# Performance work log

Measured on AMD Instinct MI355X. Metric: run time of the kernel, lower is better.

## Reference

```python
import jax, jax.numpy as jnp
import numpy as np

N = 50000      # entity nodes
E = 300000     # edges in edge_index_all (and edge_index)
E_LINE = 50000 # line-graph edges over relations
EH = 128       # e_hidden
RH = 64        # r_hidden
REL1 = 2000
REL2 = 2000
GH = 3 * EH + RH  # GAT hidden = 448


def seg_softmax(e, idx, n):
    # torch_geometric softmax: exp(e - segmax[idx]) / (segsum + 1e-16)
    m = jax.ops.segment_max(e, idx, num_segments=n)
    ex = jnp.exp(e - m[idx])
    s = jax.ops.segment_sum(ex, idx, num_segments=n)
    return ex / (s[idx] + 1e-16)


def setup_inputs() -> dict:
    key = jax.random.key(0)
    ks = jax.random.split(key, 24)

    def nrm(k, shape, s=0.1):
        return jax.random.normal(k, shape, dtype=jnp.float32) * s

    # edges without self loops: dst = (src + off) % N, off in [1, N)
    src = jax.random.randint(ks[0], (E,), 0, N)
    off = jax.random.randint(ks[1], (E,), 1, N)
    edge_index_all = jnp.stack([src, (src + off) % N])
    src2 = jax.random.randint(ks[2], (E,), 0, N)
    off2 = jax.random.randint(ks[3], (E,), 1, N)
    edge_index = jnp.stack([src2, (src2 + off2) % N])

    rel = jax.random.randint(ks[4], (E,), 0, REL1)
    rel_all = jax.random.randint(ks[5], (E,), 0, 2 * REL1)
    line_graph_index_out = jax.random.randint(ks[6], (2, E_LINE), 0, REL1)
    line_graph_index_in = jax.random.randint(ks[7], (2, E_LINE), 0, REL1)

    return {
        "x_e": nrm(ks[8], (N, EH), 1.0),
        "rel_emb1": nrm(ks[9], (REL1, RH), 1.0),
        "rel_emb2": nrm(ks[10], (REL2, RH), 1.0),
        "w_gcn1": nrm(ks[11], (EH, EH)),
        "Wh1": nrm(ks[12], (EH, EH)),
        "bh1": nrm(ks[13], (EH,)),
        "w_gcn2": nrm(ks[14], (EH, EH)),
        "Wh2": nrm(ks[15], (EH, EH)),
        "bh2": nrm(ks[16], (EH,)),
        "ai_l": nrm(ks[17], (RH,)),
        "aj_l": nrm(ks[18], (RH,)),
        "w_tw": nrm(ks[19], (2 * EH + RH,)),
        "ai_g": nrm(ks[20], (GH,)),
        "aj_g": nrm(ks[21], (GH,)),
        "ar_g": nrm(ks[22], (RH,)),
        "edge_index": edge_index,
        "rel": rel,
        "edge_index_all": edge_index_all,
        "rel_all": rel_all,
        "line_graph_index_out": line_graph_index_out,
        "line_graph_index_in": line_graph_index_in,
    }


def mrea_forward(x_e, rel_emb1, w_gcn1, Wh1, bh1, w_gcn2, Wh2, bh2,
                 ai_l, aj_l, w_tw, ai_g, aj_g, ar_g,
                 edge_index_all, rel_all, lg_out, lg_in):
    n = x_e.shape[0]
    # GCN/GAT unpack: edge_index_j, edge_index_i = edge_index (row0=j, row1=i)
    j, i = edge_index_all[0], edge_index_all[1]

    def gcn(x, W):
        deg = jax.ops.segment_sum(jnp.ones(i.shape, x.dtype), i, num_segments=n)
        dinv = jnp.where(deg > 0, deg ** -0.5, 0.0)
        norm = dinv[j] * dinv[i]  # [E]
        agg = jax.nn.relu(jax.ops.segment_sum(norm[:, None] * x[j], i, num_segments=n))
        return agg @ W.T

    def highway(x1, x2, W, b):
        g = jax.nn.sigmoid(x1 @ W.T + b)
        return g * x2 + (1.0 - g) * x1

    x = highway(x_e, gcn(x_e, w_gcn1), Wh1, bh1)
    x = highway(x, gcn(x, w_gcn2), Wh2, bh2)

    # L_GAT over relation line graphs (softmax grouped by edge_index_j, as in source)
    nr = rel_emb1.shape[0]
    def l_gat(xr, ei):
        jj, ii = ei[0], ei[1]
        e = (xr @ ai_l)[ii] + (xr @ aj_l)[jj]
        alpha = seg_softmax(jax.nn.leaky_relu(e), jj, nr)
        return jax.nn.relu(jax.ops.segment_sum(alpha[:, None] * xr[jj], ii, num_segments=nr))

    rel_emb = jnp.concatenate([l_gat(rel_emb1, lg_out), l_gat(rel_emb1, lg_in)], axis=0)  # [2*REL1, RH]

    # T-wise attention: edge_index_i, edge_index_j = edge_index_all (row0=i, row1=j)
    ti, tj = edge_index_all[0], edge_index_all[1]
    feat = jnp.concatenate([x[ti], rel_emb[rel_all], x[tj]], axis=1)  # [E, 2e+r]
    att = seg_softmax(feat @ w_tw, ti, n)
    x_agg = jax.nn.relu(jax.ops.segment_sum(feat * att[:, None], ti, num_segments=n))
    x_rel = jnp.concatenate([x, x_agg], axis=1)  # [N, 3e+r]

    # GAT on x_rel with relation bias (row0=j, row1=i)
    e = (x_rel @ ai_g)[i] + (x_rel @ aj_g)[j] + (rel_emb @ ar_g)[rel_all]
    alpha = seg_softmax(jax.nn.leaky_relu(e), i, n)
    gat_out = jax.nn.relu(jax.ops.segment_sum(alpha[:, None] * x_rel[j], i, num_segments=n))

    return jnp.concatenate([x_rel, gat_out], axis=1)  # [N, 2*(3e+r)]


def reference(x_e, rel_emb1, rel_emb2, w_gcn1, Wh1, bh1, w_gcn2, Wh2, bh2,
              ai_l, aj_l, w_tw, ai_g, aj_g, ar_g,
              edge_index, rel, edge_index_all, rel_all,
              line_graph_index_out, line_graph_index_in):
    # Branch rel.max()+1 == rel1_size is true for our data -> rel_emb1 used.
    # rel_emb2, edge_index, rel do not enter the computation on this branch.
    return mrea_forward(x_e, rel_emb1, w_gcn1, Wh1, bh1, w_gcn2, Wh2, bh2,
                        ai_l, aj_l, w_tw, ai_g, aj_g, ar_g,
                        edge_index_all, rel_all,
                        line_graph_index_out, line_graph_index_in)
```

## Files before the change

kernel.cpp:

```cpp
#include <hip/hip_runtime.h>
#include <math.h>

#define NN 50000
#define EE 300000
#define EL 50000
#define EH 128
#define RH 64
#define R1 2000
#define NR2 4000
#define OD 896
#define NT64 782
#define GCNB 12500
#define CAP 32
#define LGCAP 64

using f32x4 = __attribute__((ext_vector_type(4))) float;
using bf16x8 = __attribute__((ext_vector_type(8))) short;

__device__ __forceinline__ float leaky(float x) { return x >= 0.f ? x : 0.01f * x; }

__device__ __forceinline__ void atomicMaxF(float* addr, float val) {
    if (val >= 0.f) atomicMax((int*)addr, __float_as_int(val));
    else            atomicMin((unsigned int*)addr, __float_as_uint(val));
}

__device__ __forceinline__ short bfrn(float f) {
    unsigned u = __float_as_uint(f);
    return (short)((u + 0x7FFFu + ((u >> 16) & 1u)) >> 16);
}
__device__ __forceinline__ void cvt1(float f, short& h, short& l) {
    h = bfrn(f);
    float hf = __uint_as_float(((unsigned)(unsigned short)h) << 16);
    l = bfrn(f - hf);
}
__device__ __forceinline__ void cvt8(float4 a, float4 b, bf16x8& hi, bf16x8& lo) {
    float v[8] = {a.x, a.y, a.z, a.w, b.x, b.y, b.z, b.w};
#pragma unroll
    for (int e = 0; e < 8; ++e) {
        short h, l;
        cvt1(v[e], h, l);
        hi[e] = h;
        lo[e] = l;
    }
}

__global__ __launch_bounds__(256) void k_pre(const float* __restrict__ W0, const float* __restrict__ W1,
                                             const float* __restrict__ W2, const float* __restrict__ W3,
                                             float* __restrict__ P0, float* __restrict__ P1,
                                             float* __restrict__ P2, float* __restrict__ P3,
                                             const float* __restrict__ rel1,
                                             const float* __restrict__ ai_l, const float* __restrict__ aj_l,
                                             float* __restrict__ s_i, float* __restrict__ s_j,
                                             float* __restrict__ lgmax) {
    int b = blockIdx.x, tid = threadIdx.x;
    if (b < 32) {
        int slot = b * 256 + tid;
        int m = slot >> 11;
        int rem = slot & 2047;
        int kb = rem >> 9;
        int nt = (rem >> 6) & 7;
        int l = rem & 63;
        const float* W = m == 0 ? W0 : m == 1 ? W1 : m == 2 ? W2 : W3;
        float* P = m == 0 ? P0 : m == 1 ? P1 : m == 2 ? P2 : P3;
        int n = (nt << 4) + (l & 15);
        int k0 = (kb << 5) + ((l >> 4) << 2);
        float4 a0 = *(const float4*)(W + (n << 7) + k0);
        float4 a1 = *(const float4*)(W + (n << 7) + k0 + 16);
        bf16x8 hv, lv;
        cvt8(a0, a1, hv, lv);
        int u = ((kb << 3) + nt) * 64 + l;
        *(bf16x8*)(P + ((long)u << 2)) = hv;
        *(bf16x8*)(P + 8192 + ((long)u << 2)) = lv;
        return;
    }
    if (b < 40) {
        int r = (b - 32) * 256 + tid;
        if (r < R1) {
            const float* m = rel1 + (long)r * 64;
            float a = 0.f, bb = 0.f;
#pragma unroll
            for (int c = 0; c < 64; ++c) {
                float v = m[c];
                a += v * ai_l[c];
                bb += v * aj_l[c];
            }
            s_i[r] = a;
            s_j[r] = bb;
        }
        return;
    }
    int g = (b - 40) * 256 + tid;
    if (g < 2 * R1) lgmax[g] = -INFINITY;
}

__global__ void k_fill_all(const int* __restrict__ e0, const int* __restrict__ e1,
                           const int* __restrict__ rel_all,
                           int* __restrict__ cnt0, int* __restrict__ cnt1,
                           int2* __restrict__ csr0p, int2* __restrict__ csr1p,
                           const int* __restrict__ lgo, const int* __restrict__ lgi,
                           const float* __restrict__ s_i, const float* __restrict__ s_j,
                           float* __restrict__ lgsc, float* __restrict__ lgmax,
                           int* __restrict__ lgcnt, int* __restrict__ lgsrc,
                           int* __restrict__ lgpos) {
    int gid = blockIdx.x * blockDim.x + threadIdx.x;
    int stride = gridDim.x * blockDim.x;
    for (int i = gid; i < EE; i += stride) {
        int j0 = e0[i], i1 = e1[i], ra = rel_all[i];
        int p = atomicAdd(&cnt0[j0], 1);
        if (p < CAP) csr0p[(j0 << 5) + p] = make_int2(i1, ra);
        int q = atomicAdd(&cnt1[i1], 1);
        if (q < CAP) csr1p[(i1 << 5) + q] = make_int2(j0, ra);
    }
    for (int e = gid; e < 2 * EL; e += stride) {
        int g1 = e >= EL;
        int ee = g1 ? e - EL : e;
        const int* L = g1 ? lgi : lgo;
        int jj = L[ee], ii = L[ee + EL];
        float v = leaky(s_j[jj] + s_i[ii]);
        lgsc[e] = v;
        atomicMaxF(&lgmax[(g1 ? R1 : 0) + jj], v);
        int g = (g1 ? R1 : 0) + ii;
        int p = atomicAdd(&lgcnt[g], 1);
        if (p < LGCAP) {
            lgsrc[(g << 6) + p] = jj;
            lgpos[e] = (g << 6) + p;
        } else {
            lgpos[e] = -1;
        }
    }
}

__global__ __launch_bounds__(256) void k_dinv(const int* __restrict__ cnt1, float* __restrict__ dinv) {
    int i = blockIdx.x * 256 + threadIdx.x;
    if (i < NN) {
        int v = cnt1[i];
        dinv[i] = v > 0 ? rsqrtf((float)v) : 0.f;
    }
}

template <bool RELU>
__device__ __forceinline__ void mfma_phase(const float* __restrict__ A, const float* __restrict__ P,
                                           float4* lds4, int tid, int l, int arow, f32x4 (&acc)[8]) {
#pragma unroll
    for (int s = 0; s < 2; ++s) {
        const float* Ap = A + ((long)arow << 7) + (s << 6) + ((l >> 4) << 2);
        float4 a0 = *(const float4*)(Ap);
        float4 a1 = *(const float4*)(Ap + 16);
        float4 a2 = *(const float4*)(Ap + 32);
        float4 a3 = *(const float4*)(Ap + 48);
        if (RELU) {
            a0.x = fmaxf(a0.x, 0.f); a0.y = fmaxf(a0.y, 0.f); a0.z = fmaxf(a0.z, 0.f); a0.w = fmaxf(a0.w, 0.f);
            a1.x = fmaxf(a1.x, 0.f); a1.y = fmaxf(a1.y, 0.f); a1.z = fmaxf(a1.z, 0.f); a1.w = fmaxf(a1.w, 0.f);
            a2.x = fmaxf(a2.x, 0.f); a2.y = fmaxf(a2.y, 0.f); a2.z = fmaxf(a2.z, 0.f); a2.w = fmaxf(a2.w, 0.f);
            a3.x = fmaxf(a3.x, 0.f); a3.y = fmaxf(a3.y, 0.f); a3.z = fmaxf(a3.z, 0.f); a3.w = fmaxf(a3.w, 0.f);
        }
        __syncthreads();
        const float4* srcH = (const float4*)P + (s << 10);
        const float4* srcL = (const float4*)P + 2048 + (s << 10);
#pragma unroll
        for (int i = 0; i < 4; ++i) {
            lds4[(i << 8) + tid] = srcH[(i << 8) + tid];
            lds4[1024 + (i << 8) + tid] = srcL[(i << 8) + tid];
        }
        __syncthreads();
        bf16x8 ah0, al0, ah1, al1;
        cvt8(a0, a1, ah0, al0);
        cvt8(a2, a3, ah1, al1);
        const bf16x8* BH = (const bf16x8*)lds4;
        const bf16x8* BL = BH + 1024;
#pragma unroll
        for (int nt = 0; nt < 8; ++nt) {
            bf16x8 bh0 = BH[(nt << 6) + l];
            bf16x8 bl0 = BL[(nt << 6) + l];
            bf16x8 bh1 = BH[512 + (nt << 6) + l];
            bf16x8 bl1 = BL[512 + (nt << 6) + l];
            f32x4 c = acc[nt];
            c = __builtin_amdgcn_mfma_f32_16x16x32_bf16(ah0, bh0, c, 0, 0, 0);
            c = __builtin_amdgcn_mfma_f32_16x16x32_bf16(al0, bh0, c, 0, 0, 0);
            c = __builtin_amdgcn_mfma_f32_16x16x32_bf16(ah0, bl0, c, 0, 0, 0);
            c = __builtin_amdgcn_mfma_f32_16x16x32_bf16(ah1, bh1, c, 0, 0, 0);
            c = __builtin_amdgcn_mfma_f32_16x16x32_bf16(al1, bh1, c, 0, 0, 0);
            c = __builtin_amdgcn_mfma_f32_16x16x32_bf16(ah1, bl1, c, 0, 0, 0);
            acc[nt] = c;
        }
    }
}

template <bool XB>
__global__ __launch_bounds__(256) void k_gcn_mfma(const float* __restrict__ Agg, const float* __restrict__ Xin,
                                                  float* __restrict__ Xout,
                                                  const float* __restrict__ Pg, const float* __restrict__ Ph,
                                                  const float* __restrict__ b,
                                                  const float* __restrict__ wtw192, float* __restrict__ xb) {
    __shared__ float4 lds4[2048];
    const int tid = threadIdx.x;
    const int l = tid & 63;
    const int wv = tid >> 6;
    const int l15 = l & 15;
    const int l4 = l >> 4;
    const int rowbase = blockIdx.x * 64 + (wv << 4);
    int arow = rowbase + l15;
    if (arow >= NN) arow = NN - 1;
    f32x4 tAcc[8], hAcc[8];
#pragma unroll
    for (int nt = 0; nt < 8; ++nt) {
        tAcc[nt] = {0.f, 0.f, 0.f, 0.f};
        hAcc[nt] = {0.f, 0.f, 0.f, 0.f};
    }
    mfma_phase<true>(Agg, Pg, lds4, tid, l, arow, tAcc);
    mfma_phase<false>(Xin, Ph, lds4, tid, l, arow, hAcc);
    const int r0 = rowbase + (l4 << 2);
    float xbp[4] = {0.f, 0.f, 0.f, 0.f};
#pragma unroll
    for (int nt = 0; nt < 8; ++nt) {
        float bv = b[(nt << 4) + l15];
#pragma unroll
        for (int r = 0; r < 4; ++r) {
            int row = r0 + r;
            if (row < NN) {
                long off = ((long)row << 7) + (nt << 4) + l15;
                float xv = Xin[off];
                float g = 1.f / (1.f + expf(-(hAcc[nt][r] + bv)));
                float ov = g * tAcc[nt][r] + (1.f - g) * xv;
                Xout[off] = ov;
                if (XB) xbp[r] += ov * wtw192[(nt << 4) + l15];
            }
        }
    }
    if (XB) {
#pragma unroll
        for (int r = 0; r < 4; ++r) {
#pragma unroll
            for (int off = 1; off < 16; off <<= 1) xbp[r] += __shfl_xor(xbp[r], off);
            int row = r0 + r;
            if (l15 == 0 && row < NN) xb[row] = xbp[r];
        }
    }
}

template <int MODE>
__global__ __launch_bounds__(256) void k_gcn_gather(const int2* __restrict__ csr1p, const int* __restrict__ cnt1,
                                                    const float* __restrict__ dinv,
                                                    const float* __restrict__ x, float* __restrict__ agg,
                                                    const int* __restrict__ lgo, const int* __restrict__ lgi,
                                                    const float* __restrict__ lgsc, const float* __restrict__ lgmax,
                                                    float* __restrict__ lgsum,
                                                    const int* __restrict__ lgpos, float* __restrict__ lgscp,
                                                    const int* __restrict__ lgcnt, const int* __restrict__ lgsrc,
                                                    const float* __restrict__ rel1, float* __restrict__ relemb,
                                                    const float* __restrict__ wtw, const float* __restrict__ arg,
                                                    float* __restrict__ rw, float* __restrict__ gr) {
    if (blockIdx.x < GCNB) {
        int w = blockIdx.x * 4 + (threadIdx.x >> 6);
        int lane = threadIdx.x & 63;
        int deg = cnt1[w];
        if (deg > CAP) deg = CAP;
        int b = w << 5, en = b + deg;
        float dd = dinv[w];
        const float2* x2 = (const float2*)x;
        float2 aA = {0.f, 0.f}, aB = {0.f, 0.f}, aC = {0.f, 0.f}, aD = {0.f, 0.f};
        int idx = b;
        for (; idx + 3 < en; idx += 4) {
            int s0 = csr1p[idx].x, s1 = csr1p[idx + 1].x;
            int s2 = csr1p[idx + 2].x, s3 = csr1p[idx + 3].x;
            float w0 = dinv[s0] * dd, w1 = dinv[s1] * dd;
            float w2 = dinv[s2] * dd, w3 = dinv[s3] * dd;
            float2 v0 = x2[((long)s0 << 6) + lane];
            float2 v1 = x2[((long)s1 << 6) + lane];
            float2 v2 = x2[((long)s2 << 6) + lane];
            float2 v3 = x2[((long)s3 << 6) + lane];
            aA.x += w0 * v0.x; aA.y += w0 * v0.y;
            aB.x += w1 * v1.x; aB.y += w1 * v1.y;
            aC.x += w2 * v2.x; aC.y += w2 * v2.y;
            aD.x += w3 * v3.x; aD.y += w3 * v3.y;
        }
        for (; idx < en; ++idx) {
            int s = csr1p[idx].x;
            float w0 = dinv[s] * dd;
            float2 v0 = x2[((long)s << 6) + lane];
            aA.x += w0 * v0.x; aA.y += w0 * v0.y;
        }
        float2 r;
        r.x = (aA.x + aB.x) + (aC.x + aD.x);
        r.y = (aA.y + aB.y) + (aC.y + aD.y);
        ((float2*)agg)[((long)w << 6) + lane] = r;
        return;
    }
    if (MODE == 1) {
        int gid = (blockIdx.x - GCNB) * 256 + threadIdx.x;
        const int stride = 391 * 256;
        for (int e = gid; e < 2 * EL; e += stride) {
            int g1 = e >= EL;
            int ee = g1 ? e - EL : e;
            const int* L = g1 ? lgi : lgo;
            int jjg = (g1 ? R1 : 0) + L[ee];
            float ex = expf(lgsc[e] - lgmax[jjg]);
            int lp = lgpos[e];
            if (lp >= 0) lgscp[lp] = ex;
            atomicAdd(&lgsum[jjg], ex);
        }
    } else {
        int d = (blockIdx.x - GCNB) * 4 + (threadIdx.x >> 6);
        int lane = threadIdx.x & 63;
        if (d >= NR2) return;
        int base = d >= R1 ? R1 : 0;
        int deg = lgcnt[d];
        if (deg > LGCAP) deg = LGCAP;
        int b = d << 6, en = b + deg;
        float aA = 0.f, aB = 0.f;
        int idx = b;
        for (; idx + 1 < en; idx += 2) {
            int j0 = lgsrc[idx], j1 = lgsrc[idx + 1];
            float al0 = lgscp[idx] / (lgsum[base + j0] + 1e-16f);
            float al1 = lgscp[idx + 1] / (lgsum[base + j1] + 1e-16f);
            aA += al0 * rel1[((long)j0 << 6) + lane];
            aB += al1 * rel1[((long)j1 << 6) + lane];
        }
        if (idx < en) {
            int j0 = lgsrc[idx];
            aA += (lgscp[idx] / (lgsum[base + j0] + 1e-16f)) * rel1[((long)j0 << 6) + lane];
        }
        float v = fmaxf(aA + aB, 0.f);
        relemb[((long)d << 6) + lane] = v;
        float pa = v * wtw[128 + lane];
        float pb = v * arg[lane];
        for (int off = 32; off > 0; off >>= 1) {
            pa += __shfl_down(pa, off);
            pb += __shfl_down(pb, off);
        }
        if (lane == 0) { rw[d] = pa; gr[d] = pb; }
    }
}

__global__ __launch_bounds__(256) void k_tw_gather(const int2* __restrict__ csr0p, const int* __restrict__ cnt0,
                                                   const float* __restrict__ xb, const float* __restrict__ rw,
                                                   const float* __restrict__ x, const float* __restrict__ relemb,
                                                   const float* __restrict__ aig, const float* __restrict__ ajg,
                                                   float* __restrict__ out,
                                                   float* __restrict__ ga, float* __restrict__ gb) {
    int w = (blockIdx.x * blockDim.x + threadIdx.x) >> 6;
    int lane = threadIdx.x & 63;
    if (w >= NN) return;
    int deg = cnt0[w];
    if (deg > CAP) deg = CAP;
    int b = w << 5, en = b + deg;
    const float2* x2 = (const float2*)x;
    float2 xt = x2[((long)w << 6) + lane];
    float m = -INFINITY, sum = 0.f;
    float a2A = 0.f, a2B = 0.f;
    float2 a3A = {0.f, 0.f}, a3B = {0.f, 0.f};
    int idx = b;
    for (; idx + 1 < en; idx += 2) {
        int2 trA = csr0p[idx], trB = csr0p[idx + 1];
        float vA = xb[trA.x] + rw[trA.y];
        float vB = xb[trB.x] + rw[trB.y];
        float mn = fmaxf(vA, vB);
        if (mn > m) {
            float s = expf(m - mn);
            sum *= s; a2A *= s; a2B *= s;
            a3A.x *= s; a3A.y *= s; a3B.x *= s; a3B.y *= s;
            m = mn;
        }
        float alA = expf(vA - m), alB = expf(vB - m);
        sum += alA + alB;
        a2A += alA * relemb[((long)trA.y << 6) + lane];
        a2B += alB * relemb[((long)trB.y << 6) + lane];
        float2 xvA = x2[((long)trA.x << 6) + lane];
        float2 xvB = x2[((long)trB.x << 6) + lane];
        a3A.x += alA * xvA.x; a3A.y += alA * xvA.y;
        a3B.x += alB * xvB.x; a3B.y += alB * xvB.y;
    }
    if (idx < en) {
        int2 tr = csr0p[idx];
        float v = xb[tr.x] + rw[tr.y];
        if (v > m) {
            float s = expf(m - v);
            sum *= s; a2A *= s; a2B *= s;
            a3A.x *= s; a3A.y *= s; a3B.x *= s; a3B.y *= s;
            m = v;
        }
        float al = expf(v - m);
        sum += al;
        a2A += al * relemb[((long)tr.y << 6) + lane];
        float2 xv = x2[((long)tr.x << 6) + lane];
        a3A.x += al * xv.x; a3A.y += al * xv.y;
    }
    float r = 1.f / (sum + 1e-16f);
    float sr = sum * r;
    float2 v23;
    v23.x = fmaxf(xt.x * sr, 0.f);
    v23.y = fmaxf(xt.y * sr, 0.f);
    float v4 = fmaxf((a2A + a2B) * r, 0.f);
    float2 v56;
    v56.x = fmaxf((a3A.x + a3B.x) * r, 0.f);
    v56.y = fmaxf((a3A.y + a3B.y) * r, 0.f);
    float* o = out + (long)w * OD;
    int c2 = 2 * lane;
    *(float2*)(o + c2) = xt;
    *(float2*)(o + 128 + c2) = v23;
    o[256 + lane] = v4;
    *(float2*)(o + 320 + c2) = v56;
    float da = xt.x * aig[c2] + xt.y * aig[c2 + 1] + v23.x * aig[128 + c2] + v23.y * aig[129 + c2] +
               v4 * aig[256 + lane] + v56.x * aig[320 + c2] + v56.y * aig[321 + c2];
    float db = xt.x * ajg[c2] + xt.y * ajg[c2 + 1] + v23.x * ajg[128 + c2] + v23.y * ajg[129 + c2] +
               v4 * ajg[256 + lane] + v56.x * ajg[320 + c2] + v56.y * ajg[321 + c2];
    for (int off = 32; off > 0; off >>= 1) {
        da += __shfl_down(da, off);
        db += __shfl_down(db, off);
    }
    if (lane == 0) { ga[w] = da; gb[w] = db; }
}

__global__ __launch_bounds__(256) void k_gat_gather(const int2* __restrict__ csr1p, const int* __restrict__ cnt1,
                                                    const float* __restrict__ ga, const float* __restrict__ gb,
                                                    const float* __restrict__ gr,
                                                    const float* __restrict__ x1,
                                                    float* __restrict__ out) {
    int w = (blockIdx.x * blockDim.x + threadIdx.x) >> 6;
    int lane = threadIdx.x & 63;
    if (w >= NN) return;
    int deg = cnt1[w];
    if (deg > CAP) deg = CAP;
    int b = w << 5, en = b + deg;
    float gaw = ga[w];
    int c2 = 2 * lane;
    const float2* x12 = (const float2*)x1;
    float m = -INFINITY, sum = 0.f;
    float2 c0A = {0.f, 0.f}, c0B = {0.f, 0.f};
    float2 c2A = {0.f, 0.f}, c2B = {0.f, 0.f};
    float  c4A = 0.f, c4B = 0.f;
    float2 c5A = {0.f, 0.f}, c5B = {0.f, 0.f};
    int idx = b;
    for (; idx + 3 < en; idx += 4) {
        int2 p0 = csr1p[idx], p1 = csr1p[idx + 1], p2 = csr1p[idx + 2], p3 = csr1p[idx + 3];
        float v0 = leaky(gaw + gb[p0.x] + gr[p0.y]);
        float v1 = leaky(gaw + gb[p1.x] + gr[p1.y]);
        float v2s = leaky(gaw + gb[p2.x] + gr[p2.y]);
        float v3s = leaky(gaw + gb[p3.x] + gr[p3.y]);
        float mn = fmaxf(fmaxf(v0, v1), fmaxf(v2s, v3s));
        if (mn > m) {
            float s = expf(m - mn);
            sum *= s;
            c0A.x *= s; c0A.y *= s; c0B.x *= s; c0B.y *= s;
            c2A.x *= s; c2A.y *= s; c2B.x *= s; c2B.y *= s;
            c4A *= s; c4B *= s;
            c5A.x *= s; c5A.y *= s; c5B.x *= s; c5B.y *= s;
            m = mn;
        }
        float al0 = expf(v0 - m), al1 = expf(v1 - m), al2 = expf(v2s - m), al3 = expf(v3s - m);
        sum += (al0 + al1) + (al2 + al3);
        float2 x0 = x12[((long)p0.x << 6) + lane];
        float2 x1v = x12[((long)p1.x << 6) + lane];
        float2 x2v = x12[((long)p2.x << 6) + lane];
        float2 x3v = x12[((long)p3.x << 6) + lane];
        const float* r0 = out + (long)p0.x * OD;
        const float* r1 = out + (long)p1.x * OD;
        const float* r2 = out + (long)p2.x * OD;
        const float* r3 = out + (long)p3.x * OD;
        float  y0 = r0[256 + lane], y1 = r1[256 + lane], y2 = r2[256 + lane], y3 = r3[256 + lane];
        float2 z0 = *(const float2*)(r0 + 320 + c2);
        float2 z1 = *(const float2*)(r1 + 320 + c2);
        float2 z2 = *(const float2*)(r2 + 320 + c2);
        float2 z3 = *(const float2*)(r3 + 320 + c2);
        c0A.x += al0 * x0.x + al1 * x1v.x;  c0A.y += al0 * x0.y + al1 * x1v.y;
        c0B.x += al2 * x2v.x + al3 * x3v.x;  c0B.y += al2 * x2v.y + al3 * x3v.y;
        c2A.x += al0 * fmaxf(x0.x, 0.f) + al1 * fmaxf(x1v.x, 0.f);
        c2A.y += al0 * fmaxf(x0.y, 0.f) + al1 * fmaxf(x1v.y, 0.f);
        c2B.x += al2 * fmaxf(x2v.x, 0.f) + al3 * fmaxf(x3v.x, 0.f);
        c2B.y += al2 * fmaxf(x2v.y, 0.f) + al3 * fmaxf(x3v.y, 0.f);
        c4A += al0 * y0 + al1 * y1;
        c4B += al2 * y2 + al3 * y3;
        c5A.x += al0 * z0.x + al1 * z1.x;  c5A.y += al0 * z0.y + al1 * z1.y;
        c5B.x += al2 * z2.x + al3 * z3.x;  c5B.y += al2 * z2.y + al3 * z3.y;
    }
    for (; idx < en; ++idx) {
        int2 p = csr1p[idx];
        float v = leaky(gaw + gb[p.x] + gr[p.y]);
        if (v > m) {
            float s = expf(m - v);
            sum *= s;
            c0A.x *= s; c0A.y *= s; c0B.x *= s; c0B.y *= s;
            c2A.x *= s; c2A.y *= s; c2B.x *= s; c2B.y *= s;
            c4A *= s; c4B *= s;
            c5A.x *= s; c5A.y *= s; c5B.x *= s; c5B.y *= s;
            m = v;
        }
        float al = expf(v - m);
        sum += al;
        float2 xv = x12[((long)p.x << 6) + lane];
        const float* row = out + (long)p.x * OD;
        float  yv = row[256 + lane];
        float2 zv = *(const float2*)(row + 320 + c2);
        c0A.x += al * xv.x; c0A.y += al * xv.y;
        c2A.x += al * fmaxf(xv.x, 0.f); c2A.y += al * fmaxf(xv.y, 0.f);
        c4A += al * yv;
        c5A.x += al * zv.x; c5A.y += al * zv.y;
    }
    float r = 1.f / (sum + 1e-16f);
    float* o = out + (long)w * OD + 448;
    float2 w0, w2, w5;
    w0.x = fmaxf((c0A.x + c0B.x) * r, 0.f);
    w0.y = fmaxf((c0A.y + c0B.y) * r, 0.f);
    w2.x = fmaxf((c2A.x + c2B.x) * r, 0.f);
    w2.y = fmaxf((c2A.y + c2B.y) * r, 0.f);
    w5.x = fmaxf((c5A.x + c5B.x) * r, 0.f);
    w5.y = fmaxf((c5A.y + c5B.y) * r, 0.f);
    *(float2*)(o + c2) = w0;
    *(float2*)(o + 128 + c2) = w2;
    o[256 + lane] = fmaxf((c4A + c4B) * r, 0.f);
    *(float2*)(o + 320 + c2) = w5;
}

static inline int gs(long n) {
    long b = (n + 255) / 256;
    return (int)(b > 8192 ? 8192 : b);
}

extern "C" void kernel_launch(void* const* d_in, const int* in_sizes, int n_in,
                              void* d_out, int out_size, void* d_ws, size_t ws_size,
                              hipStream_t stream) {
    (void)in_sizes; (void)n_in; (void)out_size; (void)ws_size;

    const float* x_e   = (const float*)d_in[0];
    const float* rel1  = (const float*)d_in[1];
    const float* wgcn1 = (const float*)d_in[3];
    const float* Wh1   = (const float*)d_in[4];
    const float* bh1   = (const float*)d_in[5];
    const float* wgcn2 = (const float*)d_in[6];
    const float* Wh2   = (const float*)d_in[7];
    const float* bh2   = (const float*)d_in[8];
    const float* ai_l  = (const float*)d_in[9];
    const float* aj_l  = (const float*)d_in[10];
    const float* w_tw  = (const float*)d_in[11];
    const float* ai_g  = (const float*)d_in[12];
    const float* aj_g  = (const float*)d_in[13];
    const float* ar_g  = (const float*)d_in[14];
    const int* eia     = (const int*)d_in[17];
    const int* rel_all = (const int*)d_in[18];
    const int* lgo     = (const int*)d_in[19];
    const int* lgi     = (const int*)d_in[20];

    const int* e0 = eia;
    const int* e1 = eia + EE;

    float* out = (float*)d_out;
    float* ws  = (float*)d_ws;

    float* x1     = ws + 0;
    float* agg    = ws + 6400000;
    float* relemb = ws + 12800000;
    float* lgsum  = ws + 13056000;
    int*   cnt0   = (int*)(ws + 13060000);
    int*   cnt1   = (int*)(ws + 13110000);
    int*   lgcnt  = (int*)(ws + 13160000);
    float* lgmax  = ws + 13164000;
    float* dinv   = ws + 13168000;
    float* xb     = ws + 13218000;
    float* rw     = ws + 13268000;
    float* gr     = ws + 13272000;
    float* ga     = ws + 13276000;
    float* gb     = ws + 13326000;
    int2*  csr0p  = (int2*)(ws + 13376000);
    int2*  csr1p  = (int2*)(ws + 16576000);
    float* wt1    = ws + 19776000;
    float* wt2    = ws + 19792384;
    float* wt3    = ws + 19808768;
    float* wt4    = ws + 19825152;
    float* s_i    = ws + 19841536;
    float* s_j    = ws + 19843536;
    float* lgsc   = ws + 19845536;
    float* lgscp  = ws + 19945536;
    int*   lgsrc  = (int*)(ws + 20201536);
    int*   lgpos  = (int*)(ws + 20457536);

    hipMemsetAsync(lgsum, 0, (size_t)108000 * sizeof(float), stream);
    k_pre<<<56, 256, 0, stream>>>(wgcn1, Wh1, wgcn2, Wh2, wt1, wt2, wt3, wt4,
                                  rel1, ai_l, aj_l, s_i, s_j, lgmax);

    k_fill_all<<<gs(EE), 256, 0, stream>>>(e0, e1, rel_all, cnt0, cnt1, csr0p, csr1p,
                                           lgo, lgi, s_i, s_j, lgsc, lgmax, lgcnt, lgsrc, lgpos);
    k_dinv<<<196, 256, 0, stream>>>(cnt1, dinv);

    k_gcn_gather<1><<<GCNB + 391, 256, 0, stream>>>(csr1p, cnt1, dinv, x_e, agg,
                                                    lgo, lgi, lgsc, lgmax, lgsum,
                                                    lgpos, lgscp, lgcnt, lgsrc, rel1, relemb,
                                                    w_tw, ar_g, rw, gr);
    k_gcn_mfma<false><<<NT64, 256, 0, stream>>>(agg, x_e, x1, wt1, wt2, bh1, nullptr, nullptr);

    k_gcn_gather<2><<<GCNB + 1000, 256, 0, stream>>>(csr1p, cnt1, dinv, x1, agg,
                                                     lgo, lgi, lgsc, lgmax, lgsum,
                                                     lgpos, lgscp, lgcnt, lgsrc, rel1, relemb,
                                                     w_tw, ar_g, rw, gr);
    k_gcn_mfma<true><<<NT64, 256, 0, stream>>>(agg, x1, x1, wt3, wt4, bh2, w_tw + 192, xb);

    k_tw_gather<<<12500, 256, 0, stream>>>(csr0p, cnt0, xb, rw, x1, relemb, ai_g, aj_g, out, ga, gb);

    k_gat_gather<<<12500, 256, 0, stream>>>(csr1p, cnt1, ga, gb, gr, x1, out);
}
```

Before: 348.6 us.

## Load edge metadata lane-parallel and broadcast via shuffles; compute softmax with wave reductions

Each wave now loads its up-to-32/64 edge indices and weights in parallel, one per lane, and broadcasts them with __shfl instead of every lane reading every index serially. The segment softmax in the TW and GAT gathers becomes a wave-wide max/sum reduction, replacing the online-rescaling loop. The separate dinv kernel is removed and rsqrt of degree is computed inline. This cuts dependent scalar load latency and one launch, at the cost of extra shuffle instructions and a less unrolled GAT loop.

```diff
diff --git a/kernel.cpp b/kernel.cpp
--- a/kernel.cpp
+++ b/kernel.cpp
@@ -130,14 +130,6 @@
     }
 }
 
-__global__ __launch_bounds__(256) void k_dinv(const int* __restrict__ cnt1, float* __restrict__ dinv) {
-    int i = blockIdx.x * 256 + threadIdx.x;
-    if (i < NN) {
-        int v = cnt1[i];
-        dinv[i] = v > 0 ? rsqrtf((float)v) : 0.f;
-    }
-}
-
 template <bool RELU>
 __device__ __forceinline__ void mfma_phase(const float* __restrict__ A, const float* __restrict__ P,
                                            float4* lds4, int tid, int l, int arow, f32x4 (&acc)[8]) {
@@ -240,7 +232,6 @@
 
 template <int MODE>
 __global__ __launch_bounds__(256) void k_gcn_gather(const int2* __restrict__ csr1p, const int* __restrict__ cnt1,
-                                                    const float* __restrict__ dinv,
                                                     const float* __restrict__ x, float* __restrict__ agg,
                                                     const int* __restrict__ lgo, const int* __restrict__ lgi,
                                                     const float* __restrict__ lgsc, const float* __restrict__ lgmax,
@@ -253,18 +244,25 @@
     if (blockIdx.x < GCNB) {
         int w = blockIdx.x * 4 + (threadIdx.x >> 6);
         int lane = threadIdx.x & 63;
-        int deg = cnt1[w];
-        if (deg > CAP) deg = CAP;
-        int b = w << 5, en = b + deg;
-        float dd = dinv[w];
+        int cw = cnt1[w];
+        int deg = cw > CAP ? CAP : cw;
+        int b = w << 5;
+        float dd = cw > 0 ? rsqrtf((float)cw) : 0.f;
+        int sidx = 0;
+        float wt = 0.f;
+        if (lane < deg) {
+            sidx = csr1p[b + lane].x;
+            int cs = cnt1[sidx];
+            wt = dd * (cs > 0 ? rsqrtf((float)cs) : 0.f);
+        }
         const float2* x2 = (const float2*)x;
         float2 aA = {0.f, 0.f}, aB = {0.f, 0.f}, aC = {0.f, 0.f}, aD = {0.f, 0.f};
-        int idx = b;
-        for (; idx + 3 < en; idx += 4) {
-            int s0 = csr1p[idx].x, s1 = csr1p[idx + 1].x;
-            int s2 = csr1p[idx + 2].x, s3 = csr1p[idx + 3].x;
-            float w0 = dinv[s0] * dd, w1 = dinv[s1] * dd;
-            float w2 = dinv[s2] * dd, w3 = dinv[s3] * dd;
+        int j = 0;
+        for (; j + 3 < deg; j += 4) {
+            int s0 = __shfl(sidx, j), s1 = __shfl(sidx, j + 1);
+            int s2 = __shfl(sidx, j + 2), s3 = __shfl(sidx, j + 3);
+            float w0 = __shfl(wt, j), w1 = __shfl(wt, j + 1);
+            float w2 = __shfl(wt, j + 2), w3 = __shfl(wt, j + 3);
             float2 v0 = x2[((long)s0 << 6) + lane];
             float2 v1 = x2[((long)s1 << 6) + lane];
             float2 v2 = x2[((long)s2 << 6) + lane];
@@ -274,10 +272,10 @@
             aC.x += w2 * v2.x; aC.y += w2 * v2.y;
             aD.x += w3 * v3.x; aD.y += w3 * v3.y;
         }
-        for (; idx < en; ++idx) {
-            int s = csr1p[idx].x;
-            float w0 = dinv[s] * dd;
-            float2 v0 = x2[((long)s << 6) + lane];
+        for (; j < deg; ++j) {
+            int s0 = __shfl(sidx, j);
+            float w0 = __shfl(wt, j);
+            float2 v0 = x2[((long)s0 << 6) + lane];
             aA.x += w0 * v0.x; aA.y += w0 * v0.y;
         }
         float2 r;
@@ -304,21 +302,27 @@
         int lane = threadIdx.x & 63;
         if (d >= NR2) return;
         int base = d >= R1 ? R1 : 0;
-        int deg = lgcnt[d];
-        if (deg > LGCAP) deg = LGCAP;
-        int b = d << 6, en = b + deg;
+        int cd = lgcnt[d];
+        int deg = cd > LGCAP ? LGCAP : cd;
+        int b = d << 6;
+        int src = 0;
+        float al = 0.f;
+        if (lane < deg) {
+            src = lgsrc[b + lane];
+            al = lgscp[b + lane] / (lgsum[base + src] + 1e-16f);
+        }
         float aA = 0.f, aB = 0.f;
-        int idx = b;
-        for (; idx + 1 < en; idx += 2) {
-            int j0 = lgsrc[idx], j1 = lgsrc[idx + 1];
-            float al0 = lgscp[idx] / (lgsum[base + j0] + 1e-16f);
-            float al1 = lgscp[idx + 1] / (lgsum[base + j1] + 1e-16f);
-            aA += al0 * rel1[((long)j0 << 6) + lane];
-            aB += al1 * rel1[((long)j1 << 6) + lane];
-        }
-        if (idx < en) {
-            int j0 = lgsrc[idx];
-            aA += (lgscp[idx] / (lgsum[base + j0] + 1e-16f)) * rel1[((long)j0 << 6) + lane];
+        int j = 0;
+        for (; j + 1 < deg; j += 2) {
+            float a0 = __shfl(al, j), a1 = __shfl(al, j + 1);
+            int s0 = __shfl(src, j), s1 = __shfl(src, j + 1);
+            aA += a0 * rel1[((long)s0 << 6) + lane];
+            aB += a1 * rel1[((long)s1 << 6) + lane];
+        }
+        if (j < deg) {
+            float a0 = __shfl(al, j);
+            int s0 = __shfl(src, j);
+            aA += a0 * rel1[((long)s0 << 6) + lane];
         }
         float v = fmaxf(aA + aB, 0.f);
         relemb[((long)d << 6) + lane] = v;
@@ -341,49 +345,46 @@
     int w = (blockIdx.x * blockDim.x + threadIdx.x) >> 6;
     int lane = threadIdx.x & 63;
     if (w >= NN) return;
-    int deg = cnt0[w];
-    if (deg > CAP) deg = CAP;
-    int b = w << 5, en = b + deg;
+    int cw = cnt0[w];
+    int deg = cw > CAP ? CAP : cw;
+    int b = w << 5;
+    int trx = 0, trr = 0;
+    float v = -INFINITY;
+    if (lane < deg) {
+        int2 tr = csr0p[b + lane];
+        trx = tr.x; trr = tr.y;
+        v = xb[trx] + rw[trr];
+    }
+    float m = v;
+#pragma unroll
+    for (int off = 32; off > 0; off >>= 1) m = fmaxf(m, __shfl_xor(m, off));
+    float al = (lane < deg) ? expf(v - m) : 0.f;
+    float sum = al;
+#pragma unroll
+    for (int off = 32; off > 0; off >>= 1) sum += __shfl_xor(sum, off);
     const float2* x2 = (const float2*)x;
     float2 xt = x2[((long)w << 6) + lane];
-    float m = -INFINITY, sum = 0.f;
     float a2A = 0.f, a2B = 0.f;
     float2 a3A = {0.f, 0.f}, a3B = {0.f, 0.f};
-    int idx = b;
-    for (; idx + 1 < en; idx += 2) {
-        int2 trA = csr0p[idx], trB = csr0p[idx + 1];
-        float vA = xb[trA.x] + rw[trA.y];
-        float vB = xb[trB.x] + rw[trB.y];
-        float mn = fmaxf(vA, vB);
-        if (mn > m) {
-            float s = expf(m - mn);
-            sum *= s; a2A *= s; a2B *= s;
-            a3A.x *= s; a3A.y *= s; a3B.x *= s; a3B.y *= s;
-            m = mn;
-        }
-        float alA = expf(vA - m), alB = expf(vB - m);
-        sum += alA + alB;
-        a2A += alA * relemb[((long)trA.y << 6) + lane];
-        a2B += alB * relemb[((long)trB.y << 6) + lane];
-        float2 xvA = x2[((long)trA.x << 6) + lane];
-        float2 xvB = x2[((long)trB.x << 6) + lane];
+    int j = 0;
+    for (; j + 1 < deg; j += 2) {
+        float alA = __shfl(al, j), alB = __shfl(al, j + 1);
+        int xA = __shfl(trx, j), xB = __shfl(trx, j + 1);
+        int yA = __shfl(trr, j), yB = __shfl(trr, j + 1);
+        a2A += alA * relemb[((long)yA << 6) + lane];
+        a2B += alB * relemb[((long)yB << 6) + lane];
+        float2 xvA = x2[((long)xA << 6) + lane];
+        float2 xvB = x2[((long)xB << 6) + lane];
         a3A.x += alA * xvA.x; a3A.y += alA * xvA.y;
         a3B.x += alB * xvB.x; a3B.y += alB * xvB.y;
     }
-    if (idx < en) {
-        int2 tr = csr0p[idx];
-        float v = xb[tr.x] + rw[tr.y];
-        if (v > m) {
-            float s = expf(m - v);
-            sum *= s; a2A *= s; a2B *= s;
-            a3A.x *= s; a3A.y *= s; a3B.x *= s; a3B.y *= s;
-            m = v;
-        }
-        float al = expf(v - m);
-        sum += al;
-        a2A += al * relemb[((long)tr.y << 6) + lane];
-        float2 xv = x2[((long)tr.x << 6) + lane];
-        a3A.x += al * xv.x; a3A.y += al * xv.y;
+    if (j < deg) {
+        float alA = __shfl(al, j);
+        int xA = __shfl(trx, j);
+        int yA = __shfl(trr, j);
+        a2A += alA * relemb[((long)yA << 6) + lane];
+        float2 xvA = x2[((long)xA << 6) + lane];
+        a3A.x += alA * xvA.x; a3A.y += alA * xvA.y;
     }
     float r = 1.f / (sum + 1e-16f);
     float sr = sum * r;
@@ -419,82 +420,59 @@
     int w = (blockIdx.x * blockDim.x + threadIdx.x) >> 6;
     int lane = threadIdx.x & 63;
     if (w >= NN) return;
-    int deg = cnt1[w];
-    if (deg > CAP) deg = CAP;
-    int b = w << 5, en = b + deg;
+    int cw = cnt1[w];
+    int deg = cw > CAP ? CAP : cw;
+    int b = w << 5;
     float gaw = ga[w];
+    int px = 0;
+    float v = -INFINITY;
+    if (lane < deg) {
+        int2 p = csr1p[b + lane];
+        px = p.x;
+        v = leaky(gaw + gb[px] + gr[p.y]);
+    }
+    float m = v;
+#pragma unroll
+    for (int off = 32; off > 0; off >>= 1) m = fmaxf(m, __shfl_xor(m, off));
+    float al = (lane < deg) ? expf(v - m) : 0.f;
+    float sum = al;
+#pragma unroll
+    for (int off = 32; off > 0; off >>= 1) sum += __shfl_xor(sum, off);
     int c2 = 2 * lane;
     const float2* x12 = (const float2*)x1;
-    float m = -INFINITY, sum = 0.f;
     float2 c0A = {0.f, 0.f}, c0B = {0.f, 0.f};
     float2 c2A = {0.f, 0.f}, c2B = {0.f, 0.f};
     float  c4A = 0.f, c4B = 0.f;
     float2 c5A = {0.f, 0.f}, c5B = {0.f, 0.f};
-    int idx = b;
-    for (; idx + 3 < en; idx += 4) {
-        int2 p0 = csr1p[idx], p1 = csr1p[idx + 1], p2 = csr1p[idx + 2], p3 = csr1p[idx + 3];
-        float v0 = leaky(gaw + gb[p0.x] + gr[p0.y]);
-        float v1 = leaky(gaw + gb[p1.x] + gr[p1.y]);
-        float v2s = leaky(gaw + gb[p2.x] + gr[p2.y]);
-        float v3s = leaky(gaw + gb[p3.x] + gr[p3.y]);
-        float mn = fmaxf(fmaxf(v0, v1), fmaxf(v2s, v3s));
-        if (mn > m) {
-            float s = expf(m - mn);
-            sum *= s;
-            c0A.x *= s; c0A.y *= s; c0B.x *= s; c0B.y *= s;
-            c2A.x *= s; c2A.y *= s; c2B.x *= s; c2B.y *= s;
-            c4A *= s; c4B *= s;
-            c5A.x *= s; c5A.y *= s; c5B.x *= s; c5B.y *= s;
-            m = mn;
-        }
-        float al0 = expf(v0 - m), al1 = expf(v1 - m), al2 = expf(v2s - m), al3 = expf(v3s - m);
-        sum += (al0 + al1) + (al2 + al3);
-        float2 x0 = x12[((long)p0.x << 6) + lane];
-        float2 x1v = x12[((long)p1.x << 6) + lane];
-        float2 x2v = x12[((long)p2.x << 6) + lane];
-        float2 x3v = x12[((long)p3.x << 6) + lane];
-        const float* r0 = out + (long)p0.x * OD;
-        const float* r1 = out + (long)p1.x * OD;
-        const float* r2 = out + (long)p2.x * OD;
-        const float* r3 = out + (long)p3.x * OD;
-        float  y0 = r0[256 + lane], y1 = r1[256 + lane], y2 = r2[256 + lane], y3 = r3[256 + lane];
+    int j = 0;
+    for (; j + 1 < deg; j += 2) {
+        float al0 = __shfl(al, j), al1 = __shfl(al, j + 1);
+        int p0 = __shfl(px, j), p1 = __shfl(px, j + 1);
+        float2 x0 = x12[((long)p0 << 6) + lane];
+        float2 x1v = x12[((long)p1 << 6) + lane];
+        const float* r0 = out + (long)p0 * OD;
+        const float* r1 = out + (long)p1 * OD;
+        float  y0 = r0[256 + lane], y1 = r1[256 + lane];
         float2 z0 = *(const float2*)(r0 + 320 + c2);
         float2 z1 = *(const float2*)(r1 + 320 + c2);
-        float2 z2 = *(const float2*)(r2 + 320 + c2);
-        float2 z3 = *(const float2*)(r3 + 320 + c2);
         c0A.x += al0 * x0.x + al1 * x1v.x;  c0A.y += al0 * x0.y + al1 * x1v.y;
-        c0B.x += al2 * x2v.x + al3 * x3v.x;  c0B.y += al2 * x2v.y + al3 * x3v.y;
         c2A.x += al0 * fmaxf(x0.x, 0.f) + al1 * fmaxf(x1v.x, 0.f);
         c2A.y += al0 * fmaxf(x0.y, 0.f) + al1 * fmaxf(x1v.y, 0.f);
-        c2B.x += al2 * fmaxf(x2v.x, 0.f) + al3 * fmaxf(x3v.x, 0.f);
-        c2B.y += al2 * fmaxf(x2v.y, 0.f) + al3 * fmaxf(x3v.y, 0.f);
         c4A += al0 * y0 + al1 * y1;
-        c4B += al2 * y2 + al3 * y3;
         c5A.x += al0 * z0.x + al1 * z1.x;  c5A.y += al0 * z0.y + al1 * z1.y;
-        c5B.x += al2 * z2.x + al3 * z3.x;  c5B.y += al2 * z2.y + al3 * z3.y;
-    }
-    for (; idx < en; ++idx) {
-        int2 p = csr1p[idx];
-        float v = leaky(gaw + gb[p.x] + gr[p.y]);
-        if (v > m) {
-            float s = expf(m - v);
-            sum *= s;
-            c0A.x *= s; c0A.y *= s; c0B.x *= s; c0B.y *= s;
-            c2A.x *= s; c2A.y *= s; c2B.x *= s; c2B.y *= s;
-            c4A *= s; c4B *= s;
-            c5A.x *= s; c5A.y *= s; c5B.x *= s; c5B.y *= s;
-            m = v;
-        }
-        float al = expf(v - m);
-        sum += al;
-        float2 xv = x12[((long)p.x << 6) + lane];
-        const float* row = out + (long)p.x * OD;
+        float2 t; (void)t;
+    }
+    if (j < deg) {
+        float al0 = __shfl(al, j);
+        int p0 = __shfl(px, j);
+        float2 xv = x12[((long)p0 << 6) + lane];
+        const float* row = out + (long)p0 * OD;
         float  yv = row[256 + lane];
         float2 zv = *(const float2*)(row + 320 + c2);
-        c0A.x += al * xv.x; c0A.y += al * xv.y;
-        c2A.x += al * fmaxf(xv.x, 0.f); c2A.y += al * fmaxf(xv.y, 0.f);
-        c4A += al * yv;
-        c5A.x += al * zv.x; c5A.y += al * zv.y;
+        c0B.x += al0 * xv.x; c0B.y += al0 * xv.y;
+        c2B.x += al0 * fmaxf(xv.x, 0.f); c2B.y += al0 * fmaxf(xv.y, 0.f);
+        c4B += al0 * yv;
+        c5B.x += al0 * zv.x; c5B.y += al0 * zv.y;
     }
     float r = 1.f / (sum + 1e-16f);
     float* o = out + (long)w * OD + 448;
@@ -554,7 +532,6 @@
     int*   cnt1   = (int*)(ws + 13110000);
     int*   lgcnt  = (int*)(ws + 13160000);
     float* lgmax  = ws + 13164000;
-    float* dinv   = ws + 13168000;
     float* xb     = ws + 13218000;
     float* rw     = ws + 13268000;
     float* gr     = ws + 13272000;
@@ -579,15 +556,14 @@
 
     k_fill_all<<<gs(EE), 256, 0, stream>>>(e0, e1, rel_all, cnt0, cnt1, csr0p, csr1p,
                                            lgo, lgi, s_i, s_j, lgsc, lgmax, lgcnt, lgsrc, lgpos);
-    k_dinv<<<196, 256, 0, stream>>>(cnt1, dinv);
-
-    k_gcn_gather<1><<<GCNB + 391, 256, 0, stream>>>(csr1p, cnt1, dinv, x_e, agg,
+
+    k_gcn_gather<1><<<GCNB + 391, 256, 0, stream>>>(csr1p, cnt1, x_e, agg,
                                                     lgo, lgi, lgsc, lgmax, lgsum,
                                                     lgpos, lgscp, lgcnt, lgsrc, rel1, relemb,
                                                     w_tw, ar_g, rw, gr);
     k_gcn_mfma<false><<<NT64, 256, 0, stream>>>(agg, x_e, x1, wt1, wt2, bh1, nullptr, nullptr);
 
-    k_gcn_gather<2><<<GCNB + 1000, 256, 0, stream>>>(csr1p, cnt1, dinv, x1, agg,
+    k_gcn_gather<2><<<GCNB + 1000, 256, 0, stream>>>(csr1p, cnt1, x1, agg,
                                                      lgo, lgi, lgsc, lgmax, lgsum,
                                                      lgpos, lgscp, lgcnt, lgsrc, rel1, relemb,
                                                      w_tw, ar_g, rw, gr);
```

Result: faster. 334.5 us (-4.0%).
